# Performance work log

Measured on AMD Instinct MI355X. Metric: run time of the kernel, lower is better.

## Reference

```python
import jax, jax.numpy as jnp
import numpy as np

KH, KW = 7, 7
H, W = 4096, 4096

def setup_inputs() -> dict:
    key = jax.random.key(0)
    k1, k2 = jax.random.split(key)
    x = jax.random.normal(k1, (H, W), dtype=jnp.float32)
    weight = jax.random.normal(k2, (KH, KW), dtype=jnp.float32) * 0.001
    bias = jnp.zeros((1,), dtype=jnp.float32)
    return {"x": x, "weight": weight, "bias": bias}

def reference(x, weight, bias):
    # Single-channel valid 2D cross-correlation + scalar bias.
    # lax.conv_general_dilated performs cross-correlation (no kernel flip),
    # matching the torch loop: res[i,j] = sum(x[i:i+kh, j:j+kw] * k).
    lhs = x[None, None, :, :]            # [N=1, C=1, H, W]
    rhs = weight[None, None, :, :]       # [O=1, I=1, kh, kw]
    out = jax.lax.conv_general_dilated(
        lhs, rhs,
        window_strides=(1, 1),
        padding="VALID",
        dimension_numbers=("NCHW", "OIHW", "NCHW"),
    )
    return out[0, 0] + bias[0]           # [H-kh+1, W-kw+1]
```

## Files before the change

kernel.cpp:

```cpp
#include <hip/hip_runtime.h>
#include <stdint.h>

#define IH 4096
#define IW 4096
#define OH 4090
#define OW 4090

#define TW 256
#define NW 8
#define TH 32
#define STEPS 4
#define WIN 38
#define RING 70
#define LW 272
#define YB (TH * STEPS)

typedef float v2f __attribute__((ext_vector_type(2)));
typedef __attribute__((address_space(1))) void gas_void;
typedef __attribute__((address_space(3))) void las_void;


__device__ __forceinline__ void stage_row(const float* __restrict__ x,
                                          int iy, int slot, int tile_x0,
                                          float* smem, int tx)
{
    iy = iy < IH ? iy : IH - 1;
    const float* gr = x + ((size_t)iy << 12);
    const int c0 = tile_x0 + 4 * tx;
    float* lp = smem + slot * LW;
    __builtin_amdgcn_global_load_lds((gas_void*)(gr + c0), (las_void*)lp, 16, 0, 0);
    int c1 = tile_x0 + 256 + tx;
    c1 = c1 <= IW - 1 ? c1 : IW - 1;
    if (tx < 16)
        __builtin_amdgcn_global_load_lds((gas_void*)(gr + c1), (las_void*)(lp + 256), 4, 0, 0);
}

__global__ __launch_bounds__(512, 4) void conv7x7_ring(
    const float* __restrict__ x,
    const float* __restrict__ w,
    const float* __restrict__ bias,
    float* __restrict__ out)
{
    __shared__ float smem[RING * LW];

    const int tid = threadIdx.x;
    const int tx  = tid & 63;
    const int wv  = tid >> 6;

    int tile_x0 = blockIdx.x * TW;
    if (tile_x0 > OW - TW) tile_x0 = OW - TW;
    int y0 = blockIdx.y * YB;
    if (y0 > OH - YB) y0 = OH - YB;

    float wt[49];
#pragma unroll
    for (int k = 0; k < 49; ++k) wt[k] = w[k];
    const float b = bias[0];

#pragma unroll
    for (int rr = 0; rr < 5; ++rr) {
        const int r = wv + NW * rr;
        if (r < WIN)
            stage_row(x, y0 + r, r, tile_x0, smem, tx);
    }
    __syncthreads();

    const int lx0 = 4 * tx;
    int base_slot = 0;

#pragma unroll 1
    for (int s = 0; s < STEPS; ++s) {
        if (s + 1 < STEPS) {
#pragma unroll
            for (int j2 = 0; j2 < 4; ++j2) {
                const int j = 4 * wv + j2;
                int sl = base_slot + WIN + j;
                if (sl >= RING) sl -= RING;
                stage_row(x, y0 + TH * s + WIN + j, sl, tile_x0, smem, tx);
            }
            __builtin_amdgcn_sched_barrier(0);
        }

        float acc[4][4];
#pragma unroll
        for (int r = 0; r < 4; ++r)
#pragma unroll
            for (int c = 0; c < 4; ++c) acc[r][c] = b;

#pragma unroll
        for (int ir = 0; ir < 10; ++ir) {
            int sl = base_slot + 4 * wv + ir;
            if (sl >= RING) sl -= RING;
            const float* srow = smem + sl * LW + lx0;
            const float4 q0 = *(const float4*)(srow);
            const float4 q1 = *(const float4*)(srow + 4);
            const float4 q2 = *(const float4*)(srow + 8);
            float rb[12];
            rb[0]=q0.x; rb[1]=q0.y; rb[2]=q0.z;  rb[3]=q0.w;
            rb[4]=q1.x; rb[5]=q1.y; rb[6]=q1.z;  rb[7]=q1.w;
            rb[8]=q2.x; rb[9]=q2.y; rb[10]=q2.z; rb[11]=q2.w;

#pragma unroll
            for (int ky = 0; ky < 7; ++ky) {
                const int ry = ir - ky;
                if (ry >= 0 && ry < 4) {
#pragma unroll
                    for (int kx = 0; kx < 7; ++kx) {
                        const float ww = wt[ky * 7 + kx];
#pragma unroll
                        for (int c = 0; c < 4; ++c)
                            acc[ry][c] += ww * rb[kx + c];
                    }
                }
            }
        }

        const int ox0 = tile_x0 + lx0;
#pragma unroll
        for (int ry = 0; ry < 4; ++ry) {
            const int oy = y0 + TH * s + 4 * wv + ry;
            float* orow = out + (size_t)oy * OW + ox0;
            *(v2f*)orow       = (v2f){ acc[ry][0], acc[ry][1] };
            *(v2f*)(orow + 2) = (v2f){ acc[ry][2], acc[ry][3] };
        }

        if (s + 1 < STEPS) {
            asm volatile("s_waitcnt vmcnt(8)" ::: "memory");
            __builtin_amdgcn_sched_barrier(0);
            __builtin_amdgcn_s_barrier();
            __builtin_amdgcn_sched_barrier(0);
            asm volatile("" ::: "memory");
        }
        base_slot += TH;
        if (base_slot >= RING) base_slot -= RING;
    }
}

extern "C" void kernel_launch(void* const* d_in, const int* in_sizes, int n_in,
                              void* d_out, int out_size, void* d_ws, size_t ws_size,
                              hipStream_t stream) {
    const float* x    = (const float*)d_in[0];
    const float* w    = (const float*)d_in[1];
    const float* bias = (const float*)d_in[2];
    float* out        = (float*)d_out;

    dim3 grid((OW + TW - 1) / TW, 4096 / YB);
    conv7x7_ring<<<grid, dim3(512), 0, stream>>>(x, w, bias, out);
}
```

Before: 132.1 us.

## Give each wavefront a private LDS ring to remove block barriers

Each of four wavefronts now owns a 32-row output strip and a private 14-row LDS ring. It streams four rows per step with vmcnt waits in place of block-wide s_barrier. Output stores go through inline asm so they do not disturb the vmcnt counting. The aim is to drop cross-wave synchronization, at the cost of reloading 6 halo rows per strip and lower occupancy with 256-thread blocks. The vmcnt(16) wait relies on the private-ring loads retiring in order, which may be fragile.

After: 132.1 us. No clear change (+0.0%).

```diff
diff --git a/kernel.cpp b/kernel.cpp
--- a/kernel.cpp
+++ b/kernel.cpp
@@ -7,13 +7,14 @@
 #define OW 4090
 
 #define TW 256
-#define NW 8
-#define TH 32
-#define STEPS 4
-#define WIN 38
-#define RING 70
+#define NW 4
+#define RPW 32
+#define RSTEP 4
+#define NSTEP 8
+#define WIN 10
+#define RING 14
 #define LW 272
-#define YB (TH * STEPS)
+#define YB (NW * RPW)
 
 typedef float v2f __attribute__((ext_vector_type(2)));
 typedef __attribute__((address_space(1))) void gas_void;
@@ -22,12 +23,12 @@
 
 __device__ __forceinline__ void stage_row(const float* __restrict__ x,
                                           int iy, int slot, int tile_x0,
-                                          float* smem, int tx)
+                                          float* ring, int tx)
 {
     iy = iy < IH ? iy : IH - 1;
     const float* gr = x + ((size_t)iy << 12);
     const int c0 = tile_x0 + 4 * tx;
-    float* lp = smem + slot * LW;
+    float* lp = ring + slot * LW;
     __builtin_amdgcn_global_load_lds((gas_void*)(gr + c0), (las_void*)lp, 16, 0, 0);
     int c1 = tile_x0 + 256 + tx;
     c1 = c1 <= IW - 1 ? c1 : IW - 1;
@@ -35,13 +36,13 @@
         __builtin_amdgcn_global_load_lds((gas_void*)(gr + c1), (las_void*)(lp + 256), 4, 0, 0);
 }
 
-__global__ __launch_bounds__(512, 4) void conv7x7_ring(
+__global__ __launch_bounds__(256, 2) void conv7x7_wavering(
     const float* __restrict__ x,
     const float* __restrict__ w,
     const float* __restrict__ bias,
     float* __restrict__ out)
 {
-    __shared__ float smem[RING * LW];
+    __shared__ float smem[NW * RING * LW];
 
     const int tid = threadIdx.x;
     const int tx  = tid & 63;
@@ -52,46 +53,52 @@
     int y0 = blockIdx.y * YB;
     if (y0 > OH - YB) y0 = OH - YB;
 
+    const int strip_y0 = y0 + RPW * wv;
+    float* ring = smem + wv * (RING * LW);
+
     float wt[49];
 #pragma unroll
     for (int k = 0; k < 49; ++k) wt[k] = w[k];
     const float b = bias[0];
 
 #pragma unroll
-    for (int rr = 0; rr < 5; ++rr) {
-        const int r = wv + NW * rr;
-        if (r < WIN)
-            stage_row(x, y0 + r, r, tile_x0, smem, tx);
-    }
-    __syncthreads();
+    for (int r = 0; r < WIN; ++r)
+        stage_row(x, strip_y0 + r, r, tile_x0, ring, tx);
 
     const int lx0 = 4 * tx;
-    int base_slot = 0;
+    const int ox0 = tile_x0 + lx0;
+    int base = 0;
 
 #pragma unroll 1
-    for (int s = 0; s < STEPS; ++s) {
-        if (s + 1 < STEPS) {
+    for (int s = 0; s < NSTEP; ++s) {
+        if (s + 1 < NSTEP) {
 #pragma unroll
-            for (int j2 = 0; j2 < 4; ++j2) {
-                const int j = 4 * wv + j2;
-                int sl = base_slot + WIN + j;
+            for (int j = 0; j < RSTEP; ++j) {
+                int sl = base + WIN + j;
                 if (sl >= RING) sl -= RING;
-                stage_row(x, y0 + TH * s + WIN + j, sl, tile_x0, smem, tx);
+                stage_row(x, strip_y0 + RSTEP * s + WIN + j, sl, tile_x0, ring, tx);
             }
-            __builtin_amdgcn_sched_barrier(0);
         }
+        __builtin_amdgcn_sched_barrier(0);
 
-        float acc[4][4];
+        if (s == 0 || s == NSTEP - 1) {
+            asm volatile("s_waitcnt vmcnt(8)" ::: "memory");
+        } else {
+            asm volatile("s_waitcnt vmcnt(16)" ::: "memory");
+        }
+        __builtin_amdgcn_sched_barrier(0);
+
+        float acc[RSTEP][4];
 #pragma unroll
-        for (int r = 0; r < 4; ++r)
+        for (int r = 0; r < RSTEP; ++r)
 #pragma unroll
             for (int c = 0; c < 4; ++c) acc[r][c] = b;
 
 #pragma unroll
-        for (int ir = 0; ir < 10; ++ir) {
-            int sl = base_slot + 4 * wv + ir;
+        for (int ir = 0; ir < WIN; ++ir) {
+            int sl = base + ir;
             if (sl >= RING) sl -= RING;
-            const float* srow = smem + sl * LW + lx0;
+            const float* srow = ring + sl * LW + lx0;
             const float4 q0 = *(const float4*)(srow);
             const float4 q1 = *(const float4*)(srow + 4);
             const float4 q2 = *(const float4*)(srow + 8);
@@ -103,7 +110,7 @@
 #pragma unroll
             for (int ky = 0; ky < 7; ++ky) {
                 const int ry = ir - ky;
-                if (ry >= 0 && ry < 4) {
+                if (ry >= 0 && ry < RSTEP) {
 #pragma unroll
                     for (int kx = 0; kx < 7; ++kx) {
                         const float ww = wt[ky * 7 + kx];
@@ -115,24 +122,20 @@
             }
         }
 
-        const int ox0 = tile_x0 + lx0;
 #pragma unroll
-        for (int ry = 0; ry < 4; ++ry) {
-            const int oy = y0 + TH * s + 4 * wv + ry;
+        for (int ry = 0; ry < RSTEP; ++ry) {
+            const int oy = strip_y0 + RSTEP * s + ry;
             float* orow = out + (size_t)oy * OW + ox0;
-            *(v2f*)orow       = (v2f){ acc[ry][0], acc[ry][1] };
-            *(v2f*)(orow + 2) = (v2f){ acc[ry][2], acc[ry][3] };
+            v2f v0 = { acc[ry][0], acc[ry][1] };
+            v2f v1 = { acc[ry][2], acc[ry][3] };
+            asm volatile("global_store_dwordx2 %0, %1, off"
+                         :: "v"(orow), "v"(v0));
+            asm volatile("global_store_dwordx2 %0, %1, off"
+                         :: "v"(orow + 2), "v"(v1));
         }
 
-        if (s + 1 < STEPS) {
-            asm volatile("s_waitcnt vmcnt(8)" ::: "memory");
-            __builtin_amdgcn_sched_barrier(0);
-            __builtin_amdgcn_s_barrier();
-            __builtin_amdgcn_sched_barrier(0);
-            asm volatile("" ::: "memory");
-        }
-        base_slot += TH;
-        if (base_slot >= RING) base_slot -= RING;
+        base += RSTEP;
+        if (base >= RING) base -= RING;
     }
 }
 
@@ -145,5 +148,5 @@
     float* out        = (float*)d_out;
 
     dim3 grid((OW + TW - 1) / TW, 4096 / YB);
-    conv7x7_ring<<<grid, dim3(512), 0, stream>>>(x, w, bias, out);
+    conv7x7_wavering<<<grid, dim3(256), 0, stream>>>(x, w, bias, out);
 }
```
